# Performance work log

Hardware: AMD Instinct MI355X
Metric: run time of the kernel (lower is better)

## Reference

```python
import jax, jax.numpy as jnp
import numpy as np

B, T, F = 256, 288, 64
UNITS = [128, 64, 64, 32]
SCALE = 0.05  # small init so relu-activated recurrence stays numerically stable


def _lstm_scan(x_tbf, Wk, Wr, b):
    """Keras LSTM with activation=relu, recurrent_activation=sigmoid.
    x_tbf: [T, B, in]. Returns all hidden states [T, B, u].
    Gate order in the fused kernel is (i, f, g, o), as in Keras."""
    u = Wr.shape[0]
    bsz = x_tbf.shape[1]

    def step(carry, xt):
        h, c = carry
        z = xt @ Wk + h @ Wr + b            # [B, 4u]
        i, f, g, o = jnp.split(z, 4, axis=-1)
        i = jax.nn.sigmoid(i)
        f = jax.nn.sigmoid(f)
        g = jax.nn.relu(g)                   # cell-input activation = relu
        o = jax.nn.sigmoid(o)
        c = f * c + i * g
        h = o * jax.nn.relu(c)               # output activation = relu
        return (h, c), h

    init = (jnp.zeros((bsz, u), x_tbf.dtype), jnp.zeros((bsz, u), x_tbf.dtype))
    _, hs = jax.lax.scan(step, init, x_tbf)
    return hs  # [T, B, u]


def setup_inputs() -> dict:
    key = jax.random.key(0)
    ks = jax.random.split(key, 20)
    out = {"x": jax.random.normal(ks[0], (B, T, F), dtype=jnp.float32)}
    ins = [F] + UNITS[:-1]
    ki = 1
    for li, (din, u) in enumerate(zip(ins, UNITS), start=1):
        out[f"W{li}"] = jax.random.normal(ks[ki], (din, 4 * u), jnp.float32) * SCALE; ki += 1
        out[f"U{li}"] = jax.random.normal(ks[ki], (u, 4 * u), jnp.float32) * SCALE; ki += 1
        out[f"b{li}"] = jnp.zeros((4 * u,), jnp.float32)
    out["Wf"] = jax.random.normal(ks[ki], (UNITS[-1], 16), jnp.float32) * SCALE; ki += 1
    out["bf"] = jnp.zeros((16,), jnp.float32)
    out["Wo"] = jax.random.normal(ks[ki], (16, 1), jnp.float32) * SCALE
    out["bo"] = jnp.zeros((1,), jnp.float32)
    return out


def reference(x, W1, U1, b1, W2, U2, b2, W3, U3, b3, W4, U4, b4, Wf, bf, Wo, bo):
    # Dropout layers are identity at inference (Keras deterministic call).
    h = jnp.transpose(x, (1, 0, 2))          # [T, B, F] time-major for scan
    h = _lstm_scan(h, W1, U1, b1)            # [T, B, 128]
    h = _lstm_scan(h, W2, U2, b2)            # [T, B, 64]
    h = _lstm_scan(h, W3, U3, b3)            # [T, B, 64]
    h_last = _lstm_scan(h, W4, U4, b4)[-1]   # [B, 32] (return_sequences=False)
    fc = jax.nn.relu(h_last @ Wf + bf)       # [B, 16]
    return fc @ Wo + bo                      # [B, 1]
```

## Files before the change

kernel.cpp:

```cpp
#include <hip/hip_runtime.h>
#include <math.h>

#define TSTEPS 288
#define NTHREADS 512

typedef float f32x2 __attribute__((ext_vector_type(2)));

__device__ __forceinline__ float sigmoidf_(float x) {
    return 1.0f / (1.0f + __expf(-x));
}

__device__ __forceinline__ void pkfma(f32x2& acc, f32x2 w, f32x2 x) {
    asm("v_pk_fma_f32 %0, %1, %2, %0" : "+v"(acc) : "v"(w), "v"(x));
}

template<int NS>
__device__ __forceinline__ float allreduce_seg(float v) {
    if constexpr (NS > 1)
        v += __int_as_float(__builtin_amdgcn_update_dpp(
                0, __float_as_int(v), 0xB1, 0xF, 0xF, true));
    if constexpr (NS > 2)
        v += __int_as_float(__builtin_amdgcn_update_dpp(
                0, __float_as_int(v), 0x4E, 0xF, 0xF, true));
    if constexpr (NS > 4)
        v += __int_as_float(__builtin_amdgcn_ds_swizzle(
                __float_as_int(v), 0x101F));
    return v;
}

template<int NS, int KSEG>
__device__ __forceinline__ int perm_idx(int j) {
    return (((j % KSEG) >> 2) * NS + (j / KSEG)) * 4 + (j & 3);
}

__device__ void run_l1(const float* __restrict__ Wk, const float* __restrict__ Wr,
                       const float* __restrict__ bias, const float* __restrict__ xg,
                       float* __restrict__ seq, float* __restrict__ xh,
                       float* __restrict__ xring, int tid)
{
    constexpr int U = 128, COLS = 512, NPI = 8, NPH = 16, NP = NPI + NPH;
    const int seg = tid & 3;
    const int u   = tid >> 2;

    f32x2 w[4][NP];
#pragma unroll
    for (int q = 0; q < NPI; ++q) {
        const int k0 = seg * 16 + 2 * q;
#pragma unroll
        for (int g = 0; g < 4; ++g)
            w[g][q] = f32x2{Wk[(size_t)k0 * COLS + g * U + u],
                            Wk[(size_t)(k0 + 1) * COLS + g * U + u]};
    }
#pragma unroll
    for (int q = 0; q < NPH; ++q) {
        const int k0 = seg * 32 + 2 * q;
#pragma unroll
        for (int g = 0; g < 4; ++g)
            w[g][NPI + q] = f32x2{Wr[(size_t)k0 * COLS + g * U + u],
                                  Wr[(size_t)(k0 + 1) * COLS + g * U + u]};
    }
    float bz[4];
#pragma unroll
    for (int g = 0; g < 4; ++g) bz[g] = bias[g * U + u];
#pragma unroll
    for (int g = 0; g < 4; ++g)
#pragma unroll
        for (int q = 0; q < NP; ++q)
            asm volatile("" : "+v"(w[g][q]));

    float cst = 0.0f;

    for (int t = 0; t < TSTEPS; ++t) {
        const float* __restrict__ xr = xh + (t & 1) * 128;
        float* __restrict__ xw       = xh + ((t + 1) & 1) * 128;

        float xstage = 0.0f;
        if (tid < 64 && (t + 1) < TSTEPS) xstage = xg[(t + 1) * 64 + tid];

        f32x2 ac0 = {0.f,0.f}, ac1 = {0.f,0.f}, ac2 = {0.f,0.f}, ac3 = {0.f,0.f};

        {
            const float4* in4 = reinterpret_cast<const float4*>(xring + (t & 1) * 64) + seg;
#pragma unroll
            for (int k = 0; k < 4; ++k) {
                const float4 v = in4[k * 4];
                const f32x2 lo = {v.x, v.y}, hi = {v.z, v.w};
                pkfma(ac0, w[0][2*k],   lo); pkfma(ac0, w[0][2*k+1], hi);
                pkfma(ac1, w[1][2*k],   lo); pkfma(ac1, w[1][2*k+1], hi);
                pkfma(ac2, w[2][2*k],   lo); pkfma(ac2, w[2][2*k+1], hi);
                pkfma(ac3, w[3][2*k],   lo); pkfma(ac3, w[3][2*k+1], hi);
            }
        }
        {
            const float4* h4 = reinterpret_cast<const float4*>(xr) + seg;
#pragma unroll
            for (int k = 0; k < 8; ++k) {
                const float4 v = h4[k * 4];
                const f32x2 lo = {v.x, v.y}, hi = {v.z, v.w};
                const int pb = NPI + 2 * k;
                pkfma(ac0, w[0][pb], lo); pkfma(ac0, w[0][pb+1], hi);
                pkfma(ac1, w[1][pb], lo); pkfma(ac1, w[1][pb+1], hi);
                pkfma(ac2, w[2][pb], lo); pkfma(ac2, w[2][pb+1], hi);
                pkfma(ac3, w[3][pb], lo); pkfma(ac3, w[3][pb+1], hi);
            }
        }
        float a0 = allreduce_seg<4>(ac0[0] + ac0[1]) + bz[0];
        float a1 = allreduce_seg<4>(ac1[0] + ac1[1]) + bz[1];
        float a2 = allreduce_seg<4>(ac2[0] + ac2[1]) + bz[2];
        float a3 = allreduce_seg<4>(ac3[0] + ac3[1]) + bz[3];

        const float gi = sigmoidf_(a0);
        const float gf = sigmoidf_(a1);
        const float gg = fmaxf(a2, 0.0f);
        const float go = sigmoidf_(a3);
        cst = fmaf(gf, cst, gi * gg);
        const float h = go * fmaxf(cst, 0.0f);

        if (seg == 0) {
            const int pj = perm_idx<4, 32>(u);
            xw[pj] = h;
            seq[t * 128 + pj] = h;
        }
        if (tid < 64 && (t + 1) < TSTEPS)
            xring[((t + 1) & 1) * 64 + perm_idx<4, 16>(tid)] = xstage;
        __syncthreads();
    }
}

__device__ void fused_l2(const float* __restrict__ Wk, const float* __restrict__ Wr,
                         const float* __restrict__ bias,
                         const float* __restrict__ seq, float* __restrict__ xh2,
                         int lt)
{
    constexpr int U = 64, COLS = 256, NPI = 16, NPH = 8, NP = NPI + NPH;
    const int seg = lt & 3;
    const int u   = lt >> 2;

    f32x2 w[4][NP];
#pragma unroll
    for (int q = 0; q < NPI; ++q) {
        const int k0 = seg * 32 + 2 * q;
#pragma unroll
        for (int g = 0; g < 4; ++g)
            w[g][q] = f32x2{Wk[(size_t)k0 * COLS + g * U + u],
                            Wk[(size_t)(k0 + 1) * COLS + g * U + u]};
    }
#pragma unroll
    for (int q = 0; q < NPH; ++q) {
        const int k0 = seg * 16 + 2 * q;
#pragma unroll
        for (int g = 0; g < 4; ++g)
            w[g][NPI + q] = f32x2{Wr[(size_t)k0 * COLS + g * U + u],
                                  Wr[(size_t)(k0 + 1) * COLS + g * U + u]};
    }
    float bz[4];
#pragma unroll
    for (int g = 0; g < 4; ++g) bz[g] = bias[g * U + u];
#pragma unroll
    for (int g = 0; g < 4; ++g)
#pragma unroll
        for (int q = 0; q < NP; ++q)
            asm volatile("" : "+v"(w[g][q]));

    float cst = 0.0f;

    for (int i = 0; i < TSTEPS + 2; ++i) {
        if (i < TSTEPS) {
            f32x2 ac0 = {0.f,0.f}, ac1 = {0.f,0.f}, ac2 = {0.f,0.f}, ac3 = {0.f,0.f};
            {
                const float4* in4 = reinterpret_cast<const float4*>(seq + i * 128) + seg;
#pragma unroll
                for (int k = 0; k < 8; ++k) {
                    const float4 v = in4[k * 4];
                    const f32x2 lo = {v.x, v.y}, hi = {v.z, v.w};
                    pkfma(ac0, w[0][2*k],   lo); pkfma(ac0, w[0][2*k+1], hi);
                    pkfma(ac1, w[1][2*k],   lo); pkfma(ac1, w[1][2*k+1], hi);
                    pkfma(ac2, w[2][2*k],   lo); pkfma(ac2, w[2][2*k+1], hi);
                    pkfma(ac3, w[3][2*k],   lo); pkfma(ac3, w[3][2*k+1], hi);
                }
            }
            {
                const float4* h4 = reinterpret_cast<const float4*>(xh2 + ((i + 1) & 1) * 64) + seg;
#pragma unroll
                for (int k = 0; k < 4; ++k) {
                    const float4 v = h4[k * 4];
                    const f32x2 lo = {v.x, v.y}, hi = {v.z, v.w};
                    const int pb = NPI + 2 * k;
                    pkfma(ac0, w[0][pb], lo); pkfma(ac0, w[0][pb+1], hi);
                    pkfma(ac1, w[1][pb], lo); pkfma(ac1, w[1][pb+1], hi);
                    pkfma(ac2, w[2][pb], lo); pkfma(ac2, w[2][pb+1], hi);
                    pkfma(ac3, w[3][pb], lo); pkfma(ac3, w[3][pb+1], hi);
                }
            }
            float a0 = allreduce_seg<4>(ac0[0] + ac0[1]) + bz[0];
            float a1 = allreduce_seg<4>(ac1[0] + ac1[1]) + bz[1];
            float a2 = allreduce_seg<4>(ac2[0] + ac2[1]) + bz[2];
            float a3 = allreduce_seg<4>(ac3[0] + ac3[1]) + bz[3];

            const float gi = sigmoidf_(a0);
            const float gf = sigmoidf_(a1);
            const float gg = fmaxf(a2, 0.0f);
            const float go = sigmoidf_(a3);
            cst = fmaf(gf, cst, gi * gg);
            const float h = go * fmaxf(cst, 0.0f);

            if (seg == 0) xh2[(i & 1) * 64 + perm_idx<4, 16>(u)] = h;
        }
        __syncthreads();
    }
}

__device__ void fused_l34(const float* __restrict__ W3k, const float* __restrict__ W3r,
                          const float* __restrict__ b3,
                          const float* __restrict__ W4k, const float* __restrict__ W4r,
                          const float* __restrict__ b4,
                          const float* __restrict__ xh2, float* __restrict__ xh3,
                          float* __restrict__ xh4, int lt)
{
    const int seg3 = lt & 3,  u3 = lt >> 2;
    const int seg4 = lt & 7,  u4 = lt >> 3;

    f32x2 w3[4][16];
#pragma unroll
    for (int q = 0; q < 8; ++q) {
        const int k0 = seg3 * 16 + 2 * q;
#pragma unroll
        for (int g = 0; g < 4; ++g)
            w3[g][q] = f32x2{W3k[(size_t)k0 * 256 + g * 64 + u3],
                             W3k[(size_t)(k0 + 1) * 256 + g * 64 + u3]};
    }
#pragma unroll
    for (int q = 0; q < 8; ++q) {
        const int k0 = seg3 * 16 + 2 * q;
#pragma unroll
        for (int g = 0; g < 4; ++g)
            w3[g][8 + q] = f32x2{W3r[(size_t)k0 * 256 + g * 64 + u3],
                                 W3r[(size_t)(k0 + 1) * 256 + g * 64 + u3]};
    }
    f32x2 w4[4][6];
#pragma unroll
    for (int q = 0; q < 4; ++q) {
        const int k0 = seg4 * 8 + 2 * q;
#pragma unroll
        for (int g = 0; g < 4; ++g)
            w4[g][q] = f32x2{W4k[(size_t)k0 * 128 + g * 32 + u4],
                             W4k[(size_t)(k0 + 1) * 128 + g * 32 + u4]};
    }
#pragma unroll
    for (int q = 0; q < 2; ++q) {
        const int k0 = seg4 * 4 + 2 * q;
#pragma unroll
        for (int g = 0; g < 4; ++g)
            w4[g][4 + q] = f32x2{W4r[(size_t)k0 * 128 + g * 32 + u4],
                                 W4r[(size_t)(k0 + 1) * 128 + g * 32 + u4]};
    }
    float bz3[4], bz4[4];
#pragma unroll
    for (int g = 0; g < 4; ++g) { bz3[g] = b3[g * 64 + u3]; bz4[g] = b4[g * 32 + u4]; }
#pragma unroll
    for (int g = 0; g < 4; ++g) {
#pragma unroll
        for (int q = 0; q < 16; ++q) asm volatile("" : "+v"(w3[g][q]));
#pragma unroll
        for (int q = 0; q < 6;  ++q) asm volatile("" : "+v"(w4[g][q]));
    }

    float c3 = 0.0f, c4 = 0.0f;

    for (int i = 0; i < TSTEPS + 2; ++i) {
        if (i >= 1 && i <= TSTEPS) {
            f32x2 ac0 = {0.f,0.f}, ac1 = {0.f,0.f}, ac2 = {0.f,0.f}, ac3 = {0.f,0.f};
            {
                const float4* in4 = reinterpret_cast<const float4*>(xh2 + ((i - 1) & 1) * 64) + seg3;
#pragma unroll
                for (int k = 0; k < 4; ++k) {
                    const float4 v = in4[k * 4];
                    const f32x2 lo = {v.x, v.y}, hi = {v.z, v.w};
                    pkfma(ac0, w3[0][2*k],   lo); pkfma(ac0, w3[0][2*k+1], hi);
                    pkfma(ac1, w3[1][2*k],   lo); pkfma(ac1, w3[1][2*k+1], hi);
                    pkfma(ac2, w3[2][2*k],   lo); pkfma(ac2, w3[2][2*k+1], hi);
                    pkfma(ac3, w3[3][2*k],   lo); pkfma(ac3, w3[3][2*k+1], hi);
                }
            }
            {
                const float4* h4 = reinterpret_cast<const float4*>(xh3 + (i & 1) * 64) + seg3;
#pragma unroll
                for (int k = 0; k < 4; ++k) {
                    const float4 v = h4[k * 4];
                    const f32x2 lo = {v.x, v.y}, hi = {v.z, v.w};
                    const int pb = 8 + 2 * k;
                    pkfma(ac0, w3[0][pb], lo); pkfma(ac0, w3[0][pb+1], hi);
                    pkfma(ac1, w3[1][pb], lo); pkfma(ac1, w3[1][pb+1], hi);
                    pkfma(ac2, w3[2][pb], lo); pkfma(ac2, w3[2][pb+1], hi);
                    pkfma(ac3, w3[3][pb], lo); pkfma(ac3, w3[3][pb+1], hi);
                }
            }
            float a0 = allreduce_seg<4>(ac0[0] + ac0[1]) + bz3[0];
            float a1 = allreduce_seg<4>(ac1[0] + ac1[1]) + bz3[1];
            float a2 = allreduce_seg<4>(ac2[0] + ac2[1]) + bz3[2];
            float a3 = allreduce_seg<4>(ac3[0] + ac3[1]) + bz3[3];
            const float gi = sigmoidf_(a0);
            const float gf = sigmoidf_(a1);
            const float gg = fmaxf(a2, 0.0f);
            const float go = sigmoidf_(a3);
            c3 = fmaf(gf, c3, gi * gg);
            const float h = go * fmaxf(c3, 0.0f);
            if (seg3 == 0) xh3[((i - 1) & 1) * 64 + perm_idx<4, 16>(u3)] = h;
        }
        if (i >= 2) {
            f32x2 ac0 = {0.f,0.f}, ac1 = {0.f,0.f}, ac2 = {0.f,0.f}, ac3 = {0.f,0.f};
            {
                const float4* in4 = reinterpret_cast<const float4*>(xh3 + (i & 1) * 64);
#pragma unroll
                for (int k = 0; k < 2; ++k) {
                    const float4 v = in4[((seg4 & 1) * 2 + k) * 4 + (seg4 >> 1)];
                    const f32x2 lo = {v.x, v.y}, hi = {v.z, v.w};
                    pkfma(ac0, w4[0][2*k],   lo); pkfma(ac0, w4[0][2*k+1], hi);
                    pkfma(ac1, w4[1][2*k],   lo); pkfma(ac1, w4[1][2*k+1], hi);
                    pkfma(ac2, w4[2][2*k],   lo); pkfma(ac2, w4[2][2*k+1], hi);
                    pkfma(ac3, w4[3][2*k],   lo); pkfma(ac3, w4[3][2*k+1], hi);
                }
            }
            {
                const float4 v = reinterpret_cast<const float4*>(xh4 + ((i - 1) & 1) * 32)[seg4];
                const f32x2 lo = {v.x, v.y}, hi = {v.z, v.w};
                pkfma(ac0, w4[0][4], lo); pkfma(ac0, w4[0][5], hi);
                pkfma(ac1, w4[1][4], lo); pkfma(ac1, w4[1][5], hi);
                pkfma(ac2, w4[2][4], lo); pkfma(ac2, w4[2][5], hi);
                pkfma(ac3, w4[3][4], lo); pkfma(ac3, w4[3][5], hi);
            }
            float a0 = allreduce_seg<8>(ac0[0] + ac0[1]) + bz4[0];
            float a1 = allreduce_seg<8>(ac1[0] + ac1[1]) + bz4[1];
            float a2 = allreduce_seg<8>(ac2[0] + ac2[1]) + bz4[2];
            float a3 = allreduce_seg<8>(ac3[0] + ac3[1]) + bz4[3];
            const float gi = sigmoidf_(a0);
            const float gf = sigmoidf_(a1);
            const float gg = fmaxf(a2, 0.0f);
            const float go = sigmoidf_(a3);
            c4 = fmaf(gf, c4, gi * gg);
            const float h = go * fmaxf(c4, 0.0f);
            if (seg4 == 0) xh4[(i & 1) * 32 + u4] = h;
        }
        __syncthreads();
    }
}

extern "C" __global__ void __launch_bounds__(NTHREADS, 2)
lstm_stack_kernel(const float* __restrict__ x,
                  const float* __restrict__ W1, const float* __restrict__ U1, const float* __restrict__ b1,
                  const float* __restrict__ W2, const float* __restrict__ U2, const float* __restrict__ b2,
                  const float* __restrict__ W3, const float* __restrict__ U3, const float* __restrict__ b3,
                  const float* __restrict__ W4, const float* __restrict__ U4, const float* __restrict__ b4,
                  const float* __restrict__ Wf, const float* __restrict__ bf,
                  const float* __restrict__ Wo, const float* __restrict__ bo,
                  float* __restrict__ out)
{
    __shared__ __align__(16) float seq[TSTEPS * 128];
    __shared__ __align__(16) float xh1[2 * 128];
    __shared__ __align__(16) float xring[2 * 64];
    __shared__ __align__(16) float xh2[2 * 64];
    __shared__ __align__(16) float xh3[2 * 64];
    __shared__ __align__(16) float xh4[2 * 32];
    __shared__ __align__(16) float hbuf[16];

    const int tid = threadIdx.x;
    const float* xg = x + (size_t)blockIdx.x * TSTEPS * 64;

    if (tid < 128) xh1[tid] = 0.0f;
    if (tid < 64) {
        xring[perm_idx<4, 16>(tid)] = xg[tid];
        xh2[64 + tid] = 0.0f;
        xh3[64 + tid] = 0.0f;
    }
    if (tid < 32) xh4[32 + tid] = 0.0f;
    __syncthreads();

    run_l1(W1, U1, b1, xg, seq, xh1, xring, tid);

    if (tid < 256) fused_l2(W2, U2, b2, seq, xh2, tid);
    else           fused_l34(W3, U3, b3, W4, U4, b4, xh2, xh3, xh4, tid - 256);
    __syncthreads();

    if (tid < 16) {
        float acc = bf[tid];
#pragma unroll
        for (int k = 0; k < 32; ++k) acc = fmaf(xh4[32 + k], Wf[k * 16 + tid], acc);
        hbuf[tid] = fmaxf(acc, 0.0f);
    }
    __syncthreads();
    if (tid == 0) {
        float acc = bo[0];
#pragma unroll
        for (int k = 0; k < 16; ++k) acc = fmaf(hbuf[k], Wo[k], acc);
        out[blockIdx.x] = acc;
    }
}

extern "C" void kernel_launch(void* const* d_in, const int* in_sizes, int n_in,
                              void* d_out, int out_size, void* d_ws, size_t ws_size,
                              hipStream_t stream) {
    const float* x  = (const float*)d_in[0];
    const float* W1 = (const float*)d_in[1];
    const float* U1 = (const float*)d_in[2];
    const float* b1 = (const float*)d_in[3];
    const float* W2 = (const float*)d_in[4];
    const float* U2 = (const float*)d_in[5];
    const float* b2 = (const float*)d_in[6];
    const float* W3 = (const float*)d_in[7];
    const float* U3 = (const float*)d_in[8];
    const float* b3 = (const float*)d_in[9];
    const float* W4 = (const float*)d_in[10];
    const float* U4 = (const float*)d_in[11];
    const float* b4 = (const float*)d_in[12];
    const float* Wf = (const float*)d_in[13];
    const float* bf = (const float*)d_in[14];
    const float* Wo = (const float*)d_in[15];
    const float* bo = (const float*)d_in[16];
    float* out = (float*)d_out;

    lstm_stack_kernel<<<dim3(256), dim3(NTHREADS), 0, stream>>>(
        x, W1, U1, b1, W2, U2, b2, W3, U3, b3, W4, U4, b4, Wf, bf, Wo, bo, out);
}
```

Baseline: 576.2 us.

## Precompute input projections into global workspace and pipeline layers 2-4 wavefront

Adds a new kernel that first computes each block's layer-1 and layer-2 input projections (x·W + b) for all timesteps in a parallel pass, writes them to a global workspace, and then runs only the recurrent matvec inside the serial time loops. Layers 2, 3 and 4 are split across separate thread groups in a skewed wavefront pipeline, with layer 2 now using 2-way segment reduction. The aim is to shorten the per-step critical path of the serial recurrence. The cost is extra global-memory traffic (about 226 MB of workspace) and a dependence on the workspace being large enough, otherwise the old kernel runs as a fallback.

```diff
diff --git a/kernel.cpp b/kernel.cpp
--- a/kernel.cpp
+++ b/kernel.cpp
@@ -33,10 +33,361 @@
     return (((j % KSEG) >> 2) * NS + (j / KSEG)) * 4 + (j & 3);
 }
 
-__device__ void run_l1(const float* __restrict__ Wk, const float* __restrict__ Wr,
-                       const float* __restrict__ bias, const float* __restrict__ xg,
-                       float* __restrict__ seq, float* __restrict__ xh,
-                       float* __restrict__ xring, int tid)
+extern "C" __global__ void __launch_bounds__(NTHREADS, 2)
+lstm_v2_kernel(const float* __restrict__ x,
+               const float* __restrict__ W1, const float* __restrict__ U1, const float* __restrict__ b1,
+               const float* __restrict__ W2, const float* __restrict__ U2, const float* __restrict__ b2,
+               const float* __restrict__ W3, const float* __restrict__ U3, const float* __restrict__ b3,
+               const float* __restrict__ W4, const float* __restrict__ U4, const float* __restrict__ b4,
+               const float* __restrict__ Wf, const float* __restrict__ bf,
+               const float* __restrict__ Wo, const float* __restrict__ bo,
+               float* __restrict__ ws,
+               float* __restrict__ out)
+{
+    __shared__ __align__(16) float seq[TSTEPS * 128];
+    __shared__ __align__(16) float xh1[2 * 128];
+    __shared__ __align__(16) float xh2a[2 * 64];
+    __shared__ __align__(16) float xh2b[2 * 64];
+    __shared__ __align__(16) float xh3[2 * 64];
+    __shared__ __align__(16) float xh4[2 * 32];
+    __shared__ __align__(16) float hbuf[16];
+
+    const int tid = threadIdx.x;
+    const int b   = blockIdx.x;
+    const float* xg = x + (size_t)b * TSTEPS * 64;
+    float* zx1s = ws + (size_t)b * TSTEPS * 512;
+    float* zx2s = ws + (size_t)256 * TSTEPS * 512 + (size_t)b * TSTEPS * 256;
+
+    {
+        const int u = tid >> 2, g = tid & 3;
+        const int colW = g * 128 + u;
+        f32x2 w1r[32];
+#pragma unroll
+        for (int q = 0; q < 32; ++q)
+            w1r[q] = f32x2{W1[(size_t)(2*q) * 512 + colW],
+                           W1[(size_t)(2*q+1) * 512 + colW]};
+        const float bb = b1[colW];
+#pragma unroll
+        for (int q = 0; q < 32; ++q) asm volatile("" : "+v"(w1r[q]));
+
+        for (int t = 0; t < TSTEPS; ++t) {
+            const float4* xt = reinterpret_cast<const float4*>(xg + t * 64);
+            f32x2 acc = {bb, 0.f};
+#pragma unroll
+            for (int k4 = 0; k4 < 16; ++k4) {
+                const float4 v = xt[k4];
+                pkfma(acc, w1r[2*k4+0], f32x2{v.x, v.y});
+                pkfma(acc, w1r[2*k4+1], f32x2{v.z, v.w});
+            }
+            zx1s[t * 512 + tid] = acc[0] + acc[1];
+        }
+    }
+    if (tid < 128) xh1[tid] = 0.0f;
+    __syncthreads();
+
+    {
+        const int seg = tid & 3, u = tid >> 2;
+        f32x2 wr[4][16];
+#pragma unroll
+        for (int q = 0; q < 16; ++q) {
+            const int row = seg * 32 + 2 * q;
+#pragma unroll
+            for (int g = 0; g < 4; ++g)
+                wr[g][q] = f32x2{U1[(size_t)row * 512 + g*128 + u],
+                                 U1[(size_t)(row+1) * 512 + g*128 + u]};
+        }
+#pragma unroll
+        for (int g = 0; g < 4; ++g)
+#pragma unroll
+            for (int q = 0; q < 16; ++q) asm volatile("" : "+v"(wr[g][q]));
+
+        float cst = 0.0f;
+        const float4* zx4 = reinterpret_cast<const float4*>(zx1s);
+        float4 zxf = zx4[u];
+        for (int t = 0; t < TSTEPS; ++t) {
+            float4 zxn = zxf;
+            if (t + 1 < TSTEPS) zxn = zx4[(t + 1) * 128 + u];
+
+            const float* xr = xh1 + (t & 1) * 128;
+            f32x2 a2[4] = {f32x2{0,0}, f32x2{0,0}, f32x2{0,0}, f32x2{0,0}};
+            const float4* h4 = reinterpret_cast<const float4*>(xr) + seg;
+#pragma unroll
+            for (int k = 0; k < 8; ++k) {
+                const float4 v = h4[k * 4];
+                const f32x2 lo = {v.x, v.y}, hi = {v.z, v.w};
+                pkfma(a2[0], wr[0][2*k], lo); pkfma(a2[0], wr[0][2*k+1], hi);
+                pkfma(a2[1], wr[1][2*k], lo); pkfma(a2[1], wr[1][2*k+1], hi);
+                pkfma(a2[2], wr[2][2*k], lo); pkfma(a2[2], wr[2][2*k+1], hi);
+                pkfma(a2[3], wr[3][2*k], lo); pkfma(a2[3], wr[3][2*k+1], hi);
+            }
+            const float a0 = allreduce_seg<4>(a2[0][0] + a2[0][1]) + zxf.x;
+            const float a1 = allreduce_seg<4>(a2[1][0] + a2[1][1]) + zxf.y;
+            const float ag = allreduce_seg<4>(a2[2][0] + a2[2][1]) + zxf.z;
+            const float a3 = allreduce_seg<4>(a2[3][0] + a2[3][1]) + zxf.w;
+
+            const float gi = sigmoidf_(a0);
+            const float gf = sigmoidf_(a1);
+            const float gg = fmaxf(ag, 0.0f);
+            const float go = sigmoidf_(a3);
+            cst = fmaf(gf, cst, gi * gg);
+            const float h = go * fmaxf(cst, 0.0f);
+
+            if (seg == 0) {
+                xh1[((t + 1) & 1) * 128 + perm_idx<4, 32>(u)] = h;
+                seq[t * 128 + perm_idx<2, 64>(u)] = h;
+            }
+            zxf = zxn;
+            __syncthreads();
+        }
+    }
+
+    {
+        const int s = tid & 1, c = tid >> 1;
+        const int u = c >> 2, g = c & 3;
+        const int colW = g * 64 + u;
+        f32x2 w2r[32];
+#pragma unroll
+        for (int q = 0; q < 32; ++q) {
+            const int row = s * 64 + 2 * q;
+            w2r[q] = f32x2{W2[(size_t)row * 256 + colW],
+                           W2[(size_t)(row+1) * 256 + colW]};
+        }
+        const float bb = (s == 0) ? b2[colW] : 0.f;
+#pragma unroll
+        for (int q = 0; q < 32; ++q) asm volatile("" : "+v"(w2r[q]));
+
+        for (int t = 0; t < TSTEPS; ++t) {
+            const float4* ht = reinterpret_cast<const float4*>(seq + t * 128);
+            f32x2 acc = {bb, 0.f};
+#pragma unroll
+            for (int k4 = 0; k4 < 16; ++k4) {
+                const float4 v = ht[k4 * 2 + s];
+                pkfma(acc, w2r[2*k4+0], f32x2{v.x, v.y});
+                pkfma(acc, w2r[2*k4+1], f32x2{v.z, v.w});
+            }
+            float z = allreduce_seg<2>(acc[0] + acc[1]);
+            if (s == 0) zx2s[t * 256 + c] = z;
+        }
+    }
+    if (tid < 64) { xh2a[64 + tid] = 0.f; xh2b[64 + tid] = 0.f; xh3[64 + tid] = 0.f; }
+    if (tid < 32) xh4[32 + tid] = 0.f;
+    __syncthreads();
+
+    if (tid < 128) {
+        const int seg = tid & 1, u = tid >> 1;
+        f32x2 wr[4][16];
+#pragma unroll
+        for (int q = 0; q < 16; ++q) {
+            const int row = seg * 32 + 2 * q;
+#pragma unroll
+            for (int g = 0; g < 4; ++g)
+                wr[g][q] = f32x2{U2[(size_t)row * 256 + g*64 + u],
+                                 U2[(size_t)(row+1) * 256 + g*64 + u]};
+        }
+#pragma unroll
+        for (int g = 0; g < 4; ++g)
+#pragma unroll
+            for (int q = 0; q < 16; ++q) asm volatile("" : "+v"(wr[g][q]));
+
+        float cst = 0.0f;
+        const float4* z4 = reinterpret_cast<const float4*>(zx2s);
+        float4 zxf = z4[u];
+        for (int i = 0; i < TSTEPS + 2; ++i) {
+            float4 zxn = zxf;
+            if (i + 1 < TSTEPS) zxn = z4[(i + 1) * 64 + u];
+            if (i < TSTEPS) {
+                f32x2 a2[4] = {f32x2{0,0}, f32x2{0,0}, f32x2{0,0}, f32x2{0,0}};
+                const float4* h4 = reinterpret_cast<const float4*>(
+                    xh2a + ((i + 1) & 1) * 64);
+#pragma unroll
+                for (int k = 0; k < 8; ++k) {
+                    const float4 v = h4[k * 2 + seg];
+                    const f32x2 lo = {v.x, v.y}, hi = {v.z, v.w};
+                    pkfma(a2[0], wr[0][2*k], lo); pkfma(a2[0], wr[0][2*k+1], hi);
+                    pkfma(a2[1], wr[1][2*k], lo); pkfma(a2[1], wr[1][2*k+1], hi);
+                    pkfma(a2[2], wr[2][2*k], lo); pkfma(a2[2], wr[2][2*k+1], hi);
+                    pkfma(a2[3], wr[3][2*k], lo); pkfma(a2[3], wr[3][2*k+1], hi);
+                }
+                const float a0 = allreduce_seg<2>(a2[0][0] + a2[0][1]) + zxf.x;
+                const float a1 = allreduce_seg<2>(a2[1][0] + a2[1][1]) + zxf.y;
+                const float ag = allreduce_seg<2>(a2[2][0] + a2[2][1]) + zxf.z;
+                const float a3 = allreduce_seg<2>(a2[3][0] + a2[3][1]) + zxf.w;
+
+                const float gi = sigmoidf_(a0);
+                const float gf = sigmoidf_(a1);
+                const float gg = fmaxf(ag, 0.0f);
+                const float go = sigmoidf_(a3);
+                cst = fmaf(gf, cst, gi * gg);
+                const float h = go * fmaxf(cst, 0.0f);
+
+                if (seg == 0) {
+                    xh2a[(i & 1) * 64 + perm_idx<2, 32>(u)] = h;
+                    xh2b[(i & 1) * 64 + perm_idx<4, 16>(u)] = h;
+                }
+            }
+            zxf = zxn;
+            __syncthreads();
+        }
+    } else if (tid < 384) {
+        const int lt = tid - 128;
+        const int seg = lt & 3, u = lt >> 2;
+        f32x2 w3[4][16];
+#pragma unroll
+        for (int q = 0; q < 8; ++q) {
+            const int row = seg * 16 + 2 * q;
+#pragma unroll
+            for (int g = 0; g < 4; ++g) {
+                w3[g][q]     = f32x2{W3[(size_t)row * 256 + g*64 + u],
+                                     W3[(size_t)(row+1) * 256 + g*64 + u]};
+                w3[g][8 + q] = f32x2{U3[(size_t)row * 256 + g*64 + u],
+                                     U3[(size_t)(row+1) * 256 + g*64 + u]};
+            }
+        }
+        float bz[4];
+#pragma unroll
+        for (int g = 0; g < 4; ++g) bz[g] = b3[g * 64 + u];
+#pragma unroll
+        for (int g = 0; g < 4; ++g)
+#pragma unroll
+            for (int q = 0; q < 16; ++q) asm volatile("" : "+v"(w3[g][q]));
+
+        float cst = 0.0f;
+        for (int i = 0; i < TSTEPS + 2; ++i) {
+            if (i >= 1 && i <= TSTEPS) {
+                f32x2 a2[4] = {f32x2{0,0}, f32x2{0,0}, f32x2{0,0}, f32x2{0,0}};
+                const float4* in4 = reinterpret_cast<const float4*>(
+                    xh2b + ((i - 1) & 1) * 64);
+#pragma unroll
+                for (int k = 0; k < 4; ++k) {
+                    const float4 v = in4[k * 4 + seg];
+                    const f32x2 lo = {v.x, v.y}, hi = {v.z, v.w};
+                    pkfma(a2[0], w3[0][2*k], lo); pkfma(a2[0], w3[0][2*k+1], hi);
+                    pkfma(a2[1], w3[1][2*k], lo); pkfma(a2[1], w3[1][2*k+1], hi);
+                    pkfma(a2[2], w3[2][2*k], lo); pkfma(a2[2], w3[2][2*k+1], hi);
+                    pkfma(a2[3], w3[3][2*k], lo); pkfma(a2[3], w3[3][2*k+1], hi);
+                }
+                const float4* h4 = reinterpret_cast<const float4*>(
+                    xh3 + (i & 1) * 64);
+#pragma unroll
+                for (int k = 0; k < 4; ++k) {
+                    const float4 v = h4[k * 4 + seg];
+                    const f32x2 lo = {v.x, v.y}, hi = {v.z, v.w};
+                    const int pb = 8 + 2 * k;
+                    pkfma(a2[0], w3[0][pb], lo); pkfma(a2[0], w3[0][pb+1], hi);
+                    pkfma(a2[1], w3[1][pb], lo); pkfma(a2[1], w3[1][pb+1], hi);
+                    pkfma(a2[2], w3[2][pb], lo); pkfma(a2[2], w3[2][pb+1], hi);
+                    pkfma(a2[3], w3[3][pb], lo); pkfma(a2[3], w3[3][pb+1], hi);
+                }
+                const float a0 = allreduce_seg<4>(a2[0][0] + a2[0][1]) + bz[0];
+                const float a1 = allreduce_seg<4>(a2[1][0] + a2[1][1]) + bz[1];
+                const float ag = allreduce_seg<4>(a2[2][0] + a2[2][1]) + bz[2];
+                const float a3 = allreduce_seg<4>(a2[3][0] + a2[3][1]) + bz[3];
+
+                const float gi = sigmoidf_(a0);
+                const float gf = sigmoidf_(a1);
+                const float gg = fmaxf(ag, 0.0f);
+                const float go = sigmoidf_(a3);
+                cst = fmaf(gf, cst, gi * gg);
+                const float h = go * fmaxf(cst, 0.0f);
+
+                if (seg == 0) xh3[((i - 1) & 1) * 64 + perm_idx<4, 16>(u)] = h;
+            }
+            __syncthreads();
+        }
+    } else {
+        const int lt = tid - 384;
+        const int seg = lt & 3, u = lt >> 2;
+        f32x2 w4[4][12];
+#pragma unroll
+        for (int q = 0; q < 8; ++q) {
+            const int row = seg * 16 + 2 * q;
+#pragma unroll
+            for (int g = 0; g < 4; ++g)
+                w4[g][q] = f32x2{W4[(size_t)row * 128 + g*32 + u],
+                                 W4[(size_t)(row+1) * 128 + g*32 + u]};
+        }
+#pragma unroll
+        for (int q = 0; q < 4; ++q) {
+            const int row = seg * 8 + 2 * q;
+#pragma unroll
+            for (int g = 0; g < 4; ++g)
+                w4[g][8 + q] = f32x2{U4[(size_t)row * 128 + g*32 + u],
+                                     U4[(size_t)(row+1) * 128 + g*32 + u]};
+        }
+        float bz[4];
+#pragma unroll
+        for (int g = 0; g < 4; ++g) bz[g] = b4[g * 32 + u];
+#pragma unroll
+        for (int g = 0; g < 4; ++g)
+#pragma unroll
+            for (int q = 0; q < 12; ++q) asm volatile("" : "+v"(w4[g][q]));
+
+        float cst = 0.0f;
+        for (int i = 0; i < TSTEPS + 2; ++i) {
+            if (i >= 2) {
+                f32x2 a2[4] = {f32x2{0,0}, f32x2{0,0}, f32x2{0,0}, f32x2{0,0}};
+                const float4* in4 = reinterpret_cast<const float4*>(
+                    xh3 + (i & 1) * 64);
+#pragma unroll
+                for (int k = 0; k < 4; ++k) {
+                    const float4 v = in4[k * 4 + seg];
+                    const f32x2 lo = {v.x, v.y}, hi = {v.z, v.w};
+                    pkfma(a2[0], w4[0][2*k], lo); pkfma(a2[0], w4[0][2*k+1], hi);
+                    pkfma(a2[1], w4[1][2*k], lo); pkfma(a2[1], w4[1][2*k+1], hi);
+                    pkfma(a2[2], w4[2][2*k], lo); pkfma(a2[2], w4[2][2*k+1], hi);
+                    pkfma(a2[3], w4[3][2*k], lo); pkfma(a2[3], w4[3][2*k+1], hi);
+                }
+                const float4* h4 = reinterpret_cast<const float4*>(
+                    xh4 + ((i - 1) & 1) * 32);
+#pragma unroll
+                for (int k = 0; k < 2; ++k) {
+                    const float4 v = h4[k * 4 + seg];
+                    const f32x2 lo = {v.x, v.y}, hi = {v.z, v.w};
+                    const int pb = 8 + 2 * k;
+                    pkfma(a2[0], w4[0][pb], lo); pkfma(a2[0], w4[0][pb+1], hi);
+                    pkfma(a2[1], w4[1][pb], lo); pkfma(a2[1], w4[1][pb+1], hi);
+                    pkfma(a2[2], w4[2][pb], lo); pkfma(a2[2], w4[2][pb+1], hi);
+                    pkfma(a2[3], w4[3][pb], lo); pkfma(a2[3], w4[3][pb+1], hi);
+                }
+                const float a0 = allreduce_seg<4>(a2[0][0] + a2[0][1]) + bz[0];
+                const float a1 = allreduce_seg<4>(a2[1][0] + a2[1][1]) + bz[1];
+                const float ag = allreduce_seg<4>(a2[2][0] + a2[2][1]) + bz[2];
+                const float a3 = allreduce_seg<4>(a2[3][0] + a2[3][1]) + bz[3];
+
+                const float gi = sigmoidf_(a0);
+                const float gf = sigmoidf_(a1);
+                const float gg = fmaxf(ag, 0.0f);
+                const float go = sigmoidf_(a3);
+                cst = fmaf(gf, cst, gi * gg);
+                const float h = go * fmaxf(cst, 0.0f);
+
+                if (seg == 0) xh4[(i & 1) * 32 + perm_idx<4, 8>(u)] = h;
+            }
+            __syncthreads();
+        }
+    }
+    __syncthreads();
+
+    if (tid < 16) {
+        float acc = bf[tid];
+#pragma unroll
+        for (int k = 0; k < 32; ++k)
+            acc = fmaf(xh4[32 + perm_idx<4, 8>(k)], Wf[k * 16 + tid], acc);
+        hbuf[tid] = fmaxf(acc, 0.0f);
+    }
+    __syncthreads();
+    if (tid == 0) {
+        float acc = bo[0];
+#pragma unroll
+        for (int k = 0; k < 16; ++k) acc = fmaf(hbuf[k], Wo[k], acc);
+        out[b] = acc;
+    }
+}
+
+__device__ void run_l1_fb(const float* __restrict__ Wk, const float* __restrict__ Wr,
+                          const float* __restrict__ bias, const float* __restrict__ xg,
+                          float* __restrict__ seq, float* __restrict__ xh,
+                          float* __restrict__ xring, int tid)
 {
     constexpr int U = 128, COLS = 512, NPI = 8, NPH = 16, NP = NPI + NPH;
     const int seg = tid & 3;
@@ -78,7 +429,6 @@
         if (tid < 64 && (t + 1) < TSTEPS) xstage = xg[(t + 1) * 64 + tid];
 
         f32x2 ac0 = {0.f,0.f}, ac1 = {0.f,0.f}, ac2 = {0.f,0.f}, ac3 = {0.f,0.f};
-
         {
             const float4* in4 = reinterpret_cast<const float4*>(xring + (t & 1) * 64) + seg;
 #pragma unroll
@@ -127,10 +477,10 @@
     }
 }
 
-__device__ void fused_l2(const float* __restrict__ Wk, const float* __restrict__ Wr,
-                         const float* __restrict__ bias,
-                         const float* __restrict__ seq, float* __restrict__ xh2,
-                         int lt)
+__device__ void fused_l2_fb(const float* __restrict__ Wk, const float* __restrict__ Wr,
+                            const float* __restrict__ bias,
+                            const float* __restrict__ seq, float* __restrict__ xh2,
+                            int lt)
 {
     constexpr int U = 64, COLS = 256, NPI = 16, NPH = 8, NP = NPI + NPH;
     const int seg = lt & 3;
@@ -210,12 +560,12 @@
     }
 }
 
-__device__ void fused_l34(const float* __restrict__ W3k, const float* __restrict__ W3r,
-                          const float* __restrict__ b3,
-                          const float* __restrict__ W4k, const float* __restrict__ W4r,
-                          const float* __restrict__ b4,
-                          const float* __restrict__ xh2, float* __restrict__ xh3,
-                          float* __restrict__ xh4, int lt)
+__device__ void fused_l34_fb(const float* __restrict__ W3k, const float* __restrict__ W3r,
+                             const float* __restrict__ b3,
+                             const float* __restrict__ W4k, const float* __restrict__ W4r,
+                             const float* __restrict__ b4,
+                             const float* __restrict__ xh2, float* __restrict__ xh3,
+                             float* __restrict__ xh4, int lt)
 {
     const int seg3 = lt & 3,  u3 = lt >> 2;
     const int seg4 = lt & 7,  u4 = lt >> 3;
@@ -225,17 +575,12 @@
     for (int q = 0; q < 8; ++q) {
         const int k0 = seg3 * 16 + 2 * q;
 #pragma unroll
-        for (int g = 0; g < 4; ++g)
-            w3[g][q] = f32x2{W3k[(size_t)k0 * 256 + g * 64 + u3],
-                             W3k[(size_t)(k0 + 1) * 256 + g * 64 + u3]};
-    }
-#pragma unroll
-    for (int q = 0; q < 8; ++q) {
-        const int k0 = seg3 * 16 + 2 * q;
-#pragma unroll
-        for (int g = 0; g < 4; ++g)
+        for (int g = 0; g < 4; ++g) {
+            w3[g][q]     = f32x2{W3k[(size_t)k0 * 256 + g * 64 + u3],
+                                 W3k[(size_t)(k0 + 1) * 256 + g * 64 + u3]};
             w3[g][8 + q] = f32x2{W3r[(size_t)k0 * 256 + g * 64 + u3],
                                  W3r[(size_t)(k0 + 1) * 256 + g * 64 + u3]};
+        }
     }
     f32x2 w4[4][6];
 #pragma unroll
@@ -346,14 +691,14 @@
 }
 
 extern "C" __global__ void __launch_bounds__(NTHREADS, 2)
-lstm_stack_kernel(const float* __restrict__ x,
-                  const float* __restrict__ W1, const float* __restrict__ U1, const float* __restrict__ b1,
-                  const float* __restrict__ W2, const float* __restrict__ U2, const float* __restrict__ b2,
-                  const float* __restrict__ W3, const float* __restrict__ U3, const float* __restrict__ b3,
-                  const float* __restrict__ W4, const float* __restrict__ U4, const float* __restrict__ b4,
-                  const float* __restrict__ Wf, const float* __restrict__ bf,
-                  const float* __restrict__ Wo, const float* __restrict__ bo,
-                  float* __restrict__ out)
+lstm_fallback_kernel(const float* __restrict__ x,
+                     const float* __restrict__ W1, const float* __restrict__ U1, const float* __restrict__ b1,
+                     const float* __restrict__ W2, const float* __restrict__ U2, const float* __restrict__ b2,
+                     const float* __restrict__ W3, const float* __restrict__ U3, const float* __restrict__ b3,
+                     const float* __restrict__ W4, const float* __restrict__ U4, const float* __restrict__ b4,
+                     const float* __restrict__ Wf, const float* __restrict__ bf,
+                     const float* __restrict__ Wo, const float* __restrict__ bo,
+                     float* __restrict__ out)
 {
     __shared__ __align__(16) float seq[TSTEPS * 128];
     __shared__ __align__(16) float xh1[2 * 128];
@@ -375,10 +720,10 @@
     if (tid < 32) xh4[32 + tid] = 0.0f;
     __syncthreads();
 
-    run_l1(W1, U1, b1, xg, seq, xh1, xring, tid);
-
-    if (tid < 256) fused_l2(W2, U2, b2, seq, xh2, tid);
-    else           fused_l34(W3, U3, b3, W4, U4, b4, xh2, xh3, xh4, tid - 256);
+    run_l1_fb(W1, U1, b1, xg, seq, xh1, xring, tid);
+
+    if (tid < 256) fused_l2_fb(W2, U2, b2, seq, xh2, tid);
+    else           fused_l34_fb(W3, U3, b3, W4, U4, b4, xh2, xh3, xh4, tid - 256);
     __syncthreads();
 
     if (tid < 16) {
@@ -418,6 +763,14 @@
     const float* bo = (const float*)d_in[16];
     float* out = (float*)d_out;
 
-    lstm_stack_kernel<<<dim3(256), dim3(NTHREADS), 0, stream>>>(
-        x, W1, U1, b1, W2, U2, b2, W3, U3, b3, W4, U4, b4, Wf, bf, Wo, bo, out);
-}
+    const size_t need = ((size_t)256 * TSTEPS * 512 + (size_t)256 * TSTEPS * 256)
+                        * sizeof(float);
+    if (ws_size >= need) {
+        lstm_v2_kernel<<<dim3(256), dim3(NTHREADS), 0, stream>>>(
+            x, W1, U1, b1, W2, U2, b2, W3, U3, b3, W4, U4, b4, Wf, bf, Wo, bo,
+            (float*)d_ws, out);
+    } else {
+        lstm_fallback_kernel<<<dim3(256), dim3(NTHREADS), 0, stream>>>(
+            x, W1, U1, b1, W2, U2, b2, W3, U3, b3, W4, U4, b4, Wf, bf, Wo, bo, out);
+    }
+}
```

After: 832.5 us. 1.44x slower.
